# Kernel tuning notes

Hardware: AMD Instinct MI355X
Metric: run time of the kernel (lower is better)

## Reference

```python
import jax, jax.numpy as jnp
import numpy as np

N = 2_000_000   # points
C = 65_536      # cluster centers
F = 8           # point feature dim
D = 3           # coord dim


def _dense_params(key, din, dout):
    kw, kb = jax.random.split(key)
    scale = jnp.sqrt(2.0 / din).astype(jnp.float32)
    return (jax.random.normal(kw, (din, dout), jnp.float32) * scale,
            jnp.zeros((dout,), jnp.float32))


def setup_inputs() -> dict:
    key = jax.random.key(0)
    ks = jax.random.split(key, 16)
    inp = {
        "point_features": jax.random.normal(ks[0], (N, F), jnp.float32),
        "labels": jax.random.randint(ks[1], (N,), 0, C, jnp.int32),
        "cluster_centers": jax.random.normal(ks[2], (C, D), jnp.float32),
        "points": jax.random.normal(ks[3], (N, D), jnp.float32),
    }
    # edge MLP: (F+D)->8->16->32->64
    dims = [F + D, 8, 16, 32, 64]
    for i in range(4):
        w, b = _dense_params(ks[4 + i], dims[i], dims[i + 1])
        inp[f"we{i}"] = w
        inp[f"be{i}"] = b
    # attention MLP: (F+D)->64->1
    inp["wa0"], inp["ba0"] = _dense_params(ks[8], F + D, 64)
    inp["wa1"], inp["ba1"] = _dense_params(ks[9], 64, 1)
    # output MLP: 64->128->256
    inp["wo0"], inp["bo0"] = _dense_params(ks[10], 64, 128)
    inp["wo1"], inp["bo1"] = _dense_params(ks[11], 128, 256)
    return inp


def reference(point_features, labels, cluster_centers, points,
              we0, be0, we1, be1, we2, be2, we3, be3,
              wa0, ba0, wa1, ba1, wo0, bo0, wo1, bo1):
    relu = jax.nn.relu
    # gather center coords for each point, build edge input [N, F+D]
    center_coords = cluster_centers[labels]
    x = jnp.concatenate([point_features, center_coords - points], axis=-1)
    # edge MLP 8->16->32->64 (all relu)
    h = relu(x @ we0 + be0)
    h = relu(h @ we1 + be1)
    h = relu(h @ we2 + be2)
    h = relu(h @ we3 + be3)            # [N, 64]
    # attention MLP 64->1 sigmoid
    a = relu(x @ wa0 + ba0)
    a = jax.nn.sigmoid(a @ wa1 + ba1)  # [N, 1]
    t = h * a
    # scatter-sum into clusters
    agg = jax.ops.segment_sum(t, labels, num_segments=C)  # [C, 64]
    # output MLP 128->256 (relu, relu)
    o = relu(agg @ wo0 + bo0)
    o = relu(o @ wo1 + bo1)            # [C, 256]
    return o
```

## Files before the change

### kernel.cpp

```cpp
#include <hip/hip_runtime.h>
#include <hip/hip_bf16.h>
#include <math.h>
#include <stdint.h>

#define TPB 256
#define NCB 32
#define SAGG_LD 68
#define SMID_LD 132

__global__ __launch_bounds__(TPB) void hist_kernel(
    const int* __restrict__ labels, int* __restrict__ counts, int n)
{
    int i = blockIdx.x * TPB + threadIdx.x;
    if (i < n) atomicAdd(&counts[labels[i]], 1);
}

__global__ __launch_bounds__(256) void scan_local(
    const int* __restrict__ counts, int* __restrict__ off,
    int* __restrict__ bsum, int C)
{
    __shared__ int sh[256];
    int t = threadIdx.x;
    int i = blockIdx.x * 256 + t;
    int v = (i < C) ? counts[i] : 0;
    sh[t] = v;
    __syncthreads();
    for (int d = 1; d < 256; d <<= 1) {
        int u = (t >= d) ? sh[t - d] : 0;
        __syncthreads();
        sh[t] += u;
        __syncthreads();
    }
    if (i < C) off[i] = sh[t] - v;
    if (t == 255) bsum[blockIdx.x] = sh[255];
}

__global__ __launch_bounds__(256) void scan_base(
    int* __restrict__ bsum, int* __restrict__ off, int nb, int C)
{
    __shared__ int sh[256];
    int t = threadIdx.x;
    int v = (t < nb) ? bsum[t] : 0;
    sh[t] = v;
    __syncthreads();
    for (int d = 1; d < 256; d <<= 1) {
        int u = (t >= d) ? sh[t - d] : 0;
        __syncthreads();
        sh[t] += u;
        __syncthreads();
    }
    if (t < nb) bsum[t] = sh[t] - v;
    if (t == 255) off[C] = sh[255];
}

__global__ __launch_bounds__(256) void scan_apply(
    int* __restrict__ off, int* __restrict__ cursor,
    const int* __restrict__ bsum, int C)
{
    int i = blockIdx.x * 256 + threadIdx.x;
    if (i < C) {
        int v = off[i] + bsum[blockIdx.x];
        off[i] = v;
        cursor[i] = v;
    }
}

__global__ __launch_bounds__(TPB, 4) void point_mlp_kernel(
    const float* __restrict__ pf, const int* __restrict__ labels,
    const float* __restrict__ centers, const float* __restrict__ points,
    const float* __restrict__ we0, const float* __restrict__ be0,
    const float* __restrict__ we1, const float* __restrict__ be1,
    const float* __restrict__ we2, const float* __restrict__ be2,
    const float* __restrict__ we3, const float* __restrict__ be3,
    const float* __restrict__ wa0, const float* __restrict__ ba0,
    const float* __restrict__ wa1, const float* __restrict__ ba1,
    int* __restrict__ cursor, unsigned short* __restrict__ tsort, int n)
{
    int i = blockIdx.x * TPB + threadIdx.x;
    if (i >= n) return;

    float x[11];
    const float4* pf4 = (const float4*)pf;
    float4 p0 = pf4[(size_t)i * 2 + 0];
    float4 p1 = pf4[(size_t)i * 2 + 1];
    x[0] = p0.x; x[1] = p0.y; x[2] = p0.z; x[3] = p0.w;
    x[4] = p1.x; x[5] = p1.y; x[6] = p1.z; x[7] = p1.w;

    int lbl = labels[i];
    x[8]  = centers[lbl * 3 + 0] - points[(size_t)i * 3 + 0];
    x[9]  = centers[lbl * 3 + 1] - points[(size_t)i * 3 + 1];
    x[10] = centers[lbl * 3 + 2] - points[(size_t)i * 3 + 2];

    int pos = atomicAdd(&cursor[lbl], 1);

    float s = ba1[0];
#pragma unroll
    for (int j = 0; j < 64; j++) {
        float aj = ba0[j];
#pragma unroll
        for (int k = 0; k < 11; k++) aj = fmaf(x[k], wa0[k * 64 + j], aj);
        aj = fmaxf(aj, 0.f);
        s = fmaf(aj, wa1[j], s);
    }
    float gate = 1.f / (1.f + __expf(-s));

    float h1[8];
#pragma unroll
    for (int j = 0; j < 8; j++) {
        float v = be0[j];
#pragma unroll
        for (int k = 0; k < 11; k++) v = fmaf(x[k], we0[k * 8 + j], v);
        h1[j] = fmaxf(v, 0.f);
    }
    float h2[16];
#pragma unroll
    for (int j = 0; j < 16; j++) {
        float v = be1[j];
#pragma unroll
        for (int k = 0; k < 8; k++) v = fmaf(h1[k], we1[k * 16 + j], v);
        h2[j] = fmaxf(v, 0.f);
    }
    float h3[32];
#pragma unroll
    for (int j = 0; j < 32; j++) {
        float v = be2[j];
#pragma unroll
        for (int k = 0; k < 16; k++) v = fmaf(h2[k], we2[k * 32 + j], v);
        h3[j] = fmaxf(v, 0.f);
    }

    uint4* dst = (uint4*)(tsort + (size_t)pos * 64);
#pragma unroll
    for (int g = 0; g < 8; g++) {
        unsigned int w[4];
#pragma unroll
        for (int q = 0; q < 4; q++) {
            unsigned int packed = 0;
#pragma unroll
            for (int h = 0; h < 2; h++) {
                int j = g * 8 + q * 2 + h;
                float v = be3[j];
#pragma unroll
                for (int k = 0; k < 32; k++) v = fmaf(h3[k], we3[k * 64 + j], v);
                v = fmaxf(v, 0.f) * gate;
                __hip_bfloat16 b = __float2bfloat16(v);
                unsigned short us = *(unsigned short*)&b;
                packed |= ((unsigned int)us) << (16 * h);
            }
            w[q] = packed;
        }
        dst[g] = make_uint4(w[0], w[1], w[2], w[3]);
    }
}

__global__ __launch_bounds__(TPB) void agg_outmlp_kernel(
    const unsigned short* __restrict__ tsort,
    const int* __restrict__ off,
    const float* __restrict__ wo0, const float* __restrict__ bo0,
    const float* __restrict__ wo1, const float* __restrict__ bo1,
    float* __restrict__ out)
{
    __shared__ float s_agg[NCB * SAGG_LD];
    __shared__ float s_mid[NCB * SMID_LD];
    int tid = threadIdx.x;
    int c0 = blockIdx.x * NCB;

    {
        int lane  = tid & 63;
        int w     = tid >> 6;
        int rlane = lane >> 3;
        int word  = lane & 7;
        const uint4* t128 = (const uint4*)tsort;
#define BF_LO(u) (__uint_as_float((u) << 16))
#define BF_HI(u) (__uint_as_float((u) & 0xffff0000u))
        for (int lc = w * 8; lc < w * 8 + 8; lc++) {
            int rb = off[c0 + lc];
            int re = off[c0 + lc + 1];
            float a[8];
#pragma unroll
            for (int q = 0; q < 8; q++) a[q] = 0.f;
            for (int r = rb; r < re; r += 16) {
                int r0 = r + rlane;
                int r1 = r + 8 + rlane;
                uint4 v0 = make_uint4(0u, 0u, 0u, 0u);
                uint4 v1 = make_uint4(0u, 0u, 0u, 0u);
                if (r0 < re) v0 = t128[(size_t)r0 * 8 + word];
                if (r1 < re) v1 = t128[(size_t)r1 * 8 + word];
                a[0] += BF_LO(v0.x) + BF_LO(v1.x);
                a[1] += BF_HI(v0.x) + BF_HI(v1.x);
                a[2] += BF_LO(v0.y) + BF_LO(v1.y);
                a[3] += BF_HI(v0.y) + BF_HI(v1.y);
                a[4] += BF_LO(v0.z) + BF_LO(v1.z);
                a[5] += BF_HI(v0.z) + BF_HI(v1.z);
                a[6] += BF_LO(v0.w) + BF_LO(v1.w);
                a[7] += BF_HI(v0.w) + BF_HI(v1.w);
            }
#pragma unroll
            for (int m = 8; m < 64; m <<= 1) {
#pragma unroll
                for (int q = 0; q < 8; q++) a[q] += __shfl_xor(a[q], m, 64);
            }
            if (rlane == 0) {
                *(float4*)&s_agg[lc * SAGG_LD + word * 8 + 0] =
                    make_float4(a[0], a[1], a[2], a[3]);
                *(float4*)&s_agg[lc * SAGG_LD + word * 8 + 4] =
                    make_float4(a[4], a[5], a[6], a[7]);
            }
        }
#undef BF_LO
#undef BF_HI
    }
    __syncthreads();

    {
        int mg = tid & 15;
        int cg = tid >> 4;
        int m0 = mg * 8;
        float acc[2][8];
#pragma unroll
        for (int mi = 0; mi < 8; mi++) {
            float b = bo0[m0 + mi];
            acc[0][mi] = b;
            acc[1][mi] = b;
        }
        for (int k = 0; k < 64; k += 4) {
            float4 a0 = *(const float4*)&s_agg[(cg * 2 + 0) * SAGG_LD + k];
            float4 a1 = *(const float4*)&s_agg[(cg * 2 + 1) * SAGG_LD + k];
            float av0[4] = {a0.x, a0.y, a0.z, a0.w};
            float av1[4] = {a1.x, a1.y, a1.z, a1.w};
#pragma unroll
            for (int q = 0; q < 4; q++) {
                float4 wlo = *(const float4*)&wo0[(k + q) * 128 + m0];
                float4 whi = *(const float4*)&wo0[(k + q) * 128 + m0 + 4];
                float wv[8] = {wlo.x, wlo.y, wlo.z, wlo.w,
                               whi.x, whi.y, whi.z, whi.w};
#pragma unroll
                for (int mi = 0; mi < 8; mi++) {
                    acc[0][mi] = fmaf(av0[q], wv[mi], acc[0][mi]);
                    acc[1][mi] = fmaf(av1[q], wv[mi], acc[1][mi]);
                }
            }
        }
#pragma unroll
        for (int c = 0; c < 2; c++) {
            float4 lo = make_float4(fmaxf(acc[c][0], 0.f), fmaxf(acc[c][1], 0.f),
                                    fmaxf(acc[c][2], 0.f), fmaxf(acc[c][3], 0.f));
            float4 hi = make_float4(fmaxf(acc[c][4], 0.f), fmaxf(acc[c][5], 0.f),
                                    fmaxf(acc[c][6], 0.f), fmaxf(acc[c][7], 0.f));
            *(float4*)&s_mid[(cg * 2 + c) * SMID_LD + m0 + 0] = lo;
            *(float4*)&s_mid[(cg * 2 + c) * SMID_LD + m0 + 4] = hi;
        }
    }
    __syncthreads();

    {
        int mg = tid & 31;
        int cg = tid >> 5;
        int m0 = mg * 8;
        float acc[4][8];
#pragma unroll
        for (int mi = 0; mi < 8; mi++) {
            float b = bo1[m0 + mi];
            acc[0][mi] = b;
            acc[1][mi] = b;
            acc[2][mi] = b;
            acc[3][mi] = b;
        }
        for (int j = 0; j < 128; j += 4) {
            float4 a0 = *(const float4*)&s_mid[(cg * 4 + 0) * SMID_LD + j];
            float4 a1 = *(const float4*)&s_mid[(cg * 4 + 1) * SMID_LD + j];
            float4 a2 = *(const float4*)&s_mid[(cg * 4 + 2) * SMID_LD + j];
            float4 a3 = *(const float4*)&s_mid[(cg * 4 + 3) * SMID_LD + j];
            float av0[4] = {a0.x, a0.y, a0.z, a0.w};
            float av1[4] = {a1.x, a1.y, a1.z, a1.w};
            float av2[4] = {a2.x, a2.y, a2.z, a2.w};
            float av3[4] = {a3.x, a3.y, a3.z, a3.w};
#pragma unroll
            for (int q = 0; q < 4; q++) {
                float4 wlo = *(const float4*)&wo1[(j + q) * 256 + m0];
                float4 whi = *(const float4*)&wo1[(j + q) * 256 + m0 + 4];
                float wv[8] = {wlo.x, wlo.y, wlo.z, wlo.w,
                               whi.x, whi.y, whi.z, whi.w};
#pragma unroll
                for (int mi = 0; mi < 8; mi++) {
                    acc[0][mi] = fmaf(av0[q], wv[mi], acc[0][mi]);
                    acc[1][mi] = fmaf(av1[q], wv[mi], acc[1][mi]);
                    acc[2][mi] = fmaf(av2[q], wv[mi], acc[2][mi]);
                    acc[3][mi] = fmaf(av3[q], wv[mi], acc[3][mi]);
                }
            }
        }
#pragma unroll
        for (int c = 0; c < 4; c++) {
            float4 lo = make_float4(fmaxf(acc[c][0], 0.f), fmaxf(acc[c][1], 0.f),
                                    fmaxf(acc[c][2], 0.f), fmaxf(acc[c][3], 0.f));
            float4 hi = make_float4(fmaxf(acc[c][4], 0.f), fmaxf(acc[c][5], 0.f),
                                    fmaxf(acc[c][6], 0.f), fmaxf(acc[c][7], 0.f));
            size_t row = (size_t)(c0 + cg * 4 + c) * 256 + m0;
            *(float4*)&out[row + 0] = lo;
            *(float4*)&out[row + 4] = hi;
        }
    }
}

extern "C" void kernel_launch(void* const* d_in, const int* in_sizes, int n_in,
                              void* d_out, int out_size, void* d_ws, size_t ws_size,
                              hipStream_t stream)
{
    const float* pf      = (const float*)d_in[0];
    const int*   labels  = (const int*)d_in[1];
    const float* centers = (const float*)d_in[2];
    const float* points  = (const float*)d_in[3];
    const float* we0 = (const float*)d_in[4];
    const float* be0 = (const float*)d_in[5];
    const float* we1 = (const float*)d_in[6];
    const float* be1 = (const float*)d_in[7];
    const float* we2 = (const float*)d_in[8];
    const float* be2 = (const float*)d_in[9];
    const float* we3 = (const float*)d_in[10];
    const float* be3 = (const float*)d_in[11];
    const float* wa0 = (const float*)d_in[12];
    const float* ba0 = (const float*)d_in[13];
    const float* wa1 = (const float*)d_in[14];
    const float* ba1 = (const float*)d_in[15];
    const float* wo0 = (const float*)d_in[16];
    const float* bo0 = (const float*)d_in[17];
    const float* wo1 = (const float*)d_in[18];
    const float* bo1 = (const float*)d_in[19];
    float* out = (float*)d_out;

    int n = in_sizes[0] / 8;
    int C = in_sizes[2] / 3;

    int* counts = (int*)d_ws;
    int* cursor = counts + C;
    int* off    = cursor + C;
    int* bsum   = off + C + 1;
    uintptr_t tb = ((uintptr_t)(bsum + 256) + 255) & ~(uintptr_t)255;
    unsigned short* tsort = (unsigned short*)tb;

    hipMemsetAsync(counts, 0, (size_t)C * sizeof(int), stream);

    int pblocks = (n + TPB - 1) / TPB;
    int nb = (C + 255) / 256;
    hist_kernel<<<pblocks, TPB, 0, stream>>>(labels, counts, n);
    scan_local<<<nb, 256, 0, stream>>>(counts, off, bsum, C);
    scan_base<<<1, 256, 0, stream>>>(bsum, off, nb, C);
    scan_apply<<<nb, 256, 0, stream>>>(off, cursor, bsum, C);

    point_mlp_kernel<<<pblocks, TPB, 0, stream>>>(
        pf, labels, centers, points,
        we0, be0, we1, be1, we2, be2, we3, be3,
        wa0, ba0, wa1, ba1, cursor, tsort, n);

    agg_outmlp_kernel<<<C / NCB, TPB, 0, stream>>>(
        tsort, off, wo0, bo0, wo1, bo1, out);
}
```

Before: 597.0 us.

## Compute final edge-MLP layer with bf16 MFMA per wavefront

Replaces the per-thread scalar 32x64 final layer of the edge MLP with a 16x16x32 bf16 MFMA. Each wavefront stages its 64 points' h3 activations in shared memory as packed bf16, loads we3 fragments, and does the matmul cooperatively. Bias, relu and gate are applied afterwards, with gate and scatter position exchanged across lanes via shuffles. The aim is to cut the dominant scalar FMA work in the point kernel, at the cost of extra LDS traffic, bf16 rounding of h3 and we3, and smaller 8-byte scattered stores instead of 16-byte ones.

```diff
diff --git a/kernel.cpp b/kernel.cpp
--- a/kernel.cpp
+++ b/kernel.cpp
@@ -7,6 +7,15 @@
 #define NCB 32
 #define SAGG_LD 68
 #define SMID_LD 132
+
+typedef float f32x4 __attribute__((ext_vector_type(4)));
+typedef short bf16x8 __attribute__((ext_vector_type(8)));
+
+__device__ inline unsigned int bf16bits(float f)
+{
+    __hip_bfloat16 b = __float2bfloat16(f);
+    return (unsigned int)(*(unsigned short*)&b);
+}
 
 __global__ __launch_bounds__(TPB) void hist_kernel(
     const int* __restrict__ labels, int* __restrict__ counts, int n)
@@ -76,8 +85,10 @@
     const float* __restrict__ wa1, const float* __restrict__ ba1,
     int* __restrict__ cursor, unsigned short* __restrict__ tsort, int n)
 {
-    int i = blockIdx.x * TPB + threadIdx.x;
-    if (i >= n) return;
+    __shared__ unsigned int s_h3[4][16][64];
+
+    int i0 = blockIdx.x * TPB + threadIdx.x;
+    int i  = (i0 < n) ? i0 : (n - 1);
 
     float x[11];
     const float4* pf4 = (const float4*)pf;
@@ -91,7 +102,8 @@
     x[9]  = centers[lbl * 3 + 1] - points[(size_t)i * 3 + 1];
     x[10] = centers[lbl * 3 + 2] - points[(size_t)i * 3 + 2];
 
-    int pos = atomicAdd(&cursor[lbl], 1);
+    int pos = 0;
+    if (i0 < n) pos = atomicAdd(&cursor[lbl], 1);
 
     float s = ba1[0];
 #pragma unroll
@@ -129,27 +141,58 @@
         h3[j] = fmaxf(v, 0.f);
     }
 
-    uint4* dst = (uint4*)(tsort + (size_t)pos * 64);
-#pragma unroll
-    for (int g = 0; g < 8; g++) {
-        unsigned int w[4];
-#pragma unroll
-        for (int q = 0; q < 4; q++) {
-            unsigned int packed = 0;
-#pragma unroll
-            for (int h = 0; h < 2; h++) {
-                int j = g * 8 + q * 2 + h;
-                float v = be3[j];
-#pragma unroll
-                for (int k = 0; k < 32; k++) v = fmaf(h3[k], we3[k * 64 + j], v);
-                v = fmaxf(v, 0.f) * gate;
-                __hip_bfloat16 b = __float2bfloat16(v);
-                unsigned short us = *(unsigned short*)&b;
-                packed |= ((unsigned int)us) << (16 * h);
-            }
-            w[q] = packed;
-        }
-        dst[g] = make_uint4(w[0], w[1], w[2], w[3]);
+    int lane = threadIdx.x & 63;
+    int w    = threadIdx.x >> 6;
+    int lg   = lane >> 4;
+    int lm   = lane & 15;
+    int pbase = blockIdx.x * TPB + w * 64;
+
+#pragma unroll
+    for (int kk = 0; kk < 16; kk++) {
+        s_h3[w][kk][lane] = bf16bits(h3[2 * kk]) | (bf16bits(h3[2 * kk + 1]) << 16);
+    }
+
+    bf16x8 afrag[4];
+#pragma unroll
+    for (int mt = 0; mt < 4; mt++) {
+        union { unsigned int u[4]; bf16x8 v; } au;
+#pragma unroll
+        for (int ii = 0; ii < 4; ii++) {
+            float w0 = we3[(lg * 8 + 2 * ii + 0) * 64 + mt * 16 + lm];
+            float w1 = we3[(lg * 8 + 2 * ii + 1) * 64 + mt * 16 + lm];
+            au.u[ii] = bf16bits(w0) | (bf16bits(w1) << 16);
+        }
+        afrag[mt] = au.v;
+    }
+
+#pragma unroll
+    for (int nt = 0; nt < 4; nt++) {
+        int   spt  = nt * 16 + lm;
+        float g    = __shfl(gate, spt, 64);
+        int   ppos = __shfl(pos,  spt, 64);
+        bool  valid = (pbase + spt) < n;
+
+        union { unsigned int u[4]; bf16x8 v; } bu;
+#pragma unroll
+        for (int ii = 0; ii < 4; ii++) bu.u[ii] = s_h3[w][lg * 4 + ii][spt];
+
+#pragma unroll
+        for (int mt = 0; mt < 4; mt++) {
+            f32x4 acc = {0.f, 0.f, 0.f, 0.f};
+            acc = __builtin_amdgcn_mfma_f32_16x16x32_bf16(afrag[mt], bu.v, acc, 0, 0, 0);
+            int jb = mt * 16 + lg * 4;
+            const float4 bias = *(const float4*)&be3[jb];
+            float v0 = fmaxf(acc[0] + bias.x, 0.f) * g;
+            float v1 = fmaxf(acc[1] + bias.y, 0.f) * g;
+            float v2 = fmaxf(acc[2] + bias.z, 0.f) * g;
+            float v3 = fmaxf(acc[3] + bias.w, 0.f) * g;
+            if (valid) {
+                unsigned int d0 = bf16bits(v0) | (bf16bits(v1) << 16);
+                unsigned int d1 = bf16bits(v2) | (bf16bits(v3) << 16);
+                *(uint2*)((unsigned int*)tsort + (size_t)ppos * 32 + (jb >> 1)) =
+                    make_uint2(d0, d1);
+            }
+        }
     }
 }
 
```

After: 557.5 us. 1.07x faster.
